# Optimization experiments

Hardware: AMD Instinct MI355X
Metric: run time of the kernel (lower is better)

## Reference

```python
import jax, jax.numpy as jnp
import numpy as np

N = 8192      # total nodes
B = 8         # graphs in batch
L = 1024      # nodes per graph (max_len)
E = 262144    # edges (before self loops)
IN = 64       # in_channels
H = 8         # heads
C = 32        # hidden_channels (per-head out dim)
D = H * C     # 256, d_model
DFF = 2048    # transformer FFN dim (torch default)
NEG = -1e9


def setup_inputs() -> dict:
    key = jax.random.key(0)
    ks = jax.random.split(key, 24)
    def p(i, shape):
        return jax.random.normal(ks[i], shape, jnp.float32) * 0.02
    x = jax.random.normal(ks[0], (N, IN), jnp.float32)
    src = jax.random.randint(ks[1], (E,), 0, N)
    dst = (src // L) * L + jax.random.randint(ks[2], (E,), 0, L)  # keep edges within a graph
    edge_index = jnp.stack([src, dst]).astype(jnp.int32)
    batch = (jnp.arange(N) // L).astype(jnp.int32)
    return dict(
        x=x, edge_index=edge_index, batch=batch,
        gat_W0=p(3, (D, IN)), gat_W12=p(4, (2, D, D)),
        gat_att_src=p(5, (3, H, C)), gat_att_dst=p(6, (3, H, C)), gat_bias=p(7, (3, D)),
        tf_qkv_w=p(8, (2, 3 * D, D)), tf_qkv_b=p(9, (2, 3 * D)),
        tf_out_w=p(10, (2, D, D)), tf_out_b=p(11, (2, D)),
        tf_ln1_w=jnp.ones((2, D)), tf_ln1_b=jnp.zeros((2, D)),
        tf_ln2_w=jnp.ones((2, D)), tf_ln2_b=jnp.zeros((2, D)),
        tf_ff1_w=p(12, (2, DFF, D)), tf_ff1_b=p(13, (2, DFF)),
        tf_ff2_w=p(14, (2, D, DFF)), tf_ff2_b=p(15, (2, D)),
        pred_w=p(16, (3, D)), pred_b=p(17, (3,)),
    )


def _gat(x, src, dst, W, att_s, att_d, bias):
    # PyG GATConv, concat=True, add_self_loops (appended in caller), eval (no dropout)
    h = (x @ W.T).reshape(-1, H, C)                       # [N,H,C]
    a_s = (h * att_s).sum(-1)                             # [N,H]
    a_d = (h * att_d).sum(-1)
    e = jax.nn.leaky_relu(a_s[src] + a_d[dst], 0.2)       # [E+N,H]
    m = jax.ops.segment_max(e, dst, num_segments=N)       # per-dst softmax
    e = jnp.exp(e - m[dst])
    s = jax.ops.segment_sum(e, dst, num_segments=N)
    alpha = e / s[dst]
    out = jax.ops.segment_sum(h[src] * alpha[..., None], dst, num_segments=N)
    return out.reshape(-1, D) + bias


def _ln(x, w, b):
    mu = x.mean(-1, keepdims=True)
    v = ((x - mu) ** 2).mean(-1, keepdims=True)
    return (x - mu) / jnp.sqrt(v + 1e-5) * w + b


def _tf_layer(x, mask, qkv_w, qkv_b, out_w, out_b, ln1w, ln1b, ln2w, ln2b, f1w, f1b, f2w, f2b):
    # torch TransformerEncoderLayer (post-LN, relu), key padding mask, eval mode
    qkv = x @ qkv_w.T + qkv_b                              # [B,L,3D]
    q, k, v = jnp.split(qkv, 3, -1)
    sh = lambda t: t.reshape(B, L, H, D // H)
    q, k, v = sh(q), sh(k), sh(v)
    sc = jnp.einsum('bqhd,bkhd->bhqk', q, k) * (1.0 / float(np.sqrt(D // H)))
    sc = jnp.where(mask[:, None, None, :], NEG, sc)
    a = jax.nn.softmax(sc, -1)
    o = jnp.einsum('bhqk,bkhd->bqhd', a, v).reshape(B, L, D)
    x = _ln(x + o @ out_w.T + out_b, ln1w, ln1b)
    f = jax.nn.relu(x @ f1w.T + f1b) @ f2w.T + f2b
    return _ln(x + f, ln2w, ln2b)


def reference(x, edge_index, batch, gat_W0, gat_W12, gat_att_src, gat_att_dst, gat_bias,
              tf_qkv_w, tf_qkv_b, tf_out_w, tf_out_b, tf_ln1_w, tf_ln1_b, tf_ln2_w, tf_ln2_b,
              tf_ff1_w, tf_ff1_b, tf_ff2_w, tf_ff2_b, pred_w, pred_b):
    loops = jnp.arange(N, dtype=edge_index.dtype)
    src = jnp.concatenate([edge_index[0], loops])
    dst = jnp.concatenate([edge_index[1], loops])
    h = jax.nn.relu(_gat(x, src, dst, gat_W0, gat_att_src[0], gat_att_dst[0], gat_bias[0]))
    for i in range(2):
        h = jax.nn.relu(_gat(h, src, dst, gat_W12[i], gat_att_src[i + 1], gat_att_dst[i + 1], gat_bias[i + 1]))
    # ragged -> padded [B, L, D] (vectorized scatter instead of python loop)
    seq_lens = jax.ops.segment_sum(jnp.ones(N, jnp.int32), batch, num_segments=B)
    starts = jnp.cumsum(seq_lens) - seq_lens
    pos = jnp.arange(N) - starts[batch]
    xp = jnp.zeros((B, L, D), h.dtype).at[batch, pos].set(h)
    mask = jnp.arange(L)[None, :] >= seq_lens[:, None]     # True = padded key
    for i in range(2):
        xp = _tf_layer(xp, mask, tf_qkv_w[i], tf_qkv_b[i], tf_out_w[i], tf_out_b[i],
                       tf_ln1_w[i], tf_ln1_b[i], tf_ln2_w[i], tf_ln2_b[i],
                       tf_ff1_w[i], tf_ff1_b[i], tf_ff2_w[i], tf_ff2_b[i])
    return xp @ pred_w.T + pred_b                          # [B,L,3]
```

## Files before the change

kernel.cpp:

```cpp
#include <hip/hip_runtime.h>
#include <hip/hip_bf16.h>

#define NN 8192
#define EE 262144
#define BB 8
#define LL 1024
#define HH 8
#define DD 256
#define DFFN 2048

typedef short s8v __attribute__((ext_vector_type(8)));
typedef float f32x4 __attribute__((ext_vector_type(4)));
typedef unsigned short ushort;

__device__ inline ushort f2bf(float f) {
    unsigned u = __float_as_uint(f);
    u = (u + 0x7fffu + ((u >> 16) & 1u)) >> 16;
    return (ushort)u;
}
__device__ inline float bf2f(ushort u) {
    return __uint_as_float(((unsigned)u) << 16);
}

__global__ __launch_bounds__(256) void mgemm_ff1_kernel(
    const ushort* __restrict__ A, const ushort* __restrict__ W,
    const float* __restrict__ bias, ushort* __restrict__ Cb,
    int M, int N, int K)
{
    __shared__ ushort As[2][128 * 64];
    __shared__ ushort Bs[2][128 * 64];
    int t = threadIdx.x;
    int l = t & 63;
    int quad = l >> 4, l15 = l & 15;
    int r7 = l15 & 7;
    int w = t >> 6;
    int wm = (w >> 1) * 64, wn = (w & 1) * 64;
    int m0 = blockIdx.x * 128, n0 = blockIdx.y * 128;

    int goffA[4], goffB[4], lo[4];
#pragma unroll
    for (int i = 0; i < 4; ++i) {
        int chunk = i * 256 + t;
        int r = chunk >> 3, p = chunk & 7;
        int qs = (p ^ (r & 7)) * 8;
        goffA[i] = (m0 + r) * K + qs;
        goffB[i] = (n0 + r) * K + qs;
        lo[i] = chunk * 8;
    }

#define STAGE_F(k0, bf)                                                         \
    {                                                                           \
        _Pragma("unroll")                                                       \
        for (int i = 0; i < 4; ++i) {                                           \
            __builtin_amdgcn_global_load_lds(                                   \
                (const __attribute__((address_space(1))) unsigned int*)         \
                    (A + goffA[i] + (k0)),                                      \
                (__attribute__((address_space(3))) unsigned int*)(&As[bf][0] + lo[i]), 16, 0, 0); \
            __builtin_amdgcn_global_load_lds(                                   \
                (const __attribute__((address_space(1))) unsigned int*)         \
                    (W + goffB[i] + (k0)),                                      \
                (__attribute__((address_space(3))) unsigned int*)(&Bs[bf][0] + lo[i]), 16, 0, 0); \
        }                                                                       \
    }

    f32x4 z = {0.f, 0.f, 0.f, 0.f};
    f32x4 acc[4][4];
#pragma unroll
    for (int i = 0; i < 4; ++i)
#pragma unroll
        for (int j = 0; j < 4; ++j) acc[i][j] = z;

    int nt = K >> 6;
    STAGE_F(0, 0);
    for (int ks = 0; ks < nt; ++ks) {
        int cur = ks & 1;
        if (ks + 1 < nt) {
            STAGE_F((ks + 1) << 6, cur ^ 1);
            asm volatile("s_waitcnt vmcnt(8)" ::: "memory");
        } else {
            asm volatile("s_waitcnt vmcnt(0)" ::: "memory");
        }
        __builtin_amdgcn_s_barrier();
        __builtin_amdgcn_sched_barrier(0);
#pragma unroll
        for (int kk = 0; kk < 2; ++kk) {
            int off = ((kk * 4 + quad) ^ r7) * 8;
            s8v af[4], bfv[4];
#pragma unroll
            for (int i = 0; i < 4; ++i) {
                af[i]  = *(const s8v*)(&As[cur][0] + (wm + i * 16 + l15) * 64 + off);
                bfv[i] = *(const s8v*)(&Bs[cur][0] + (wn + i * 16 + l15) * 64 + off);
            }
#pragma unroll
            for (int mi = 0; mi < 4; ++mi)
#pragma unroll
                for (int ni = 0; ni < 4; ++ni)
                    acc[mi][ni] = __builtin_amdgcn_mfma_f32_16x16x32_bf16(
                        af[mi], bfv[ni], acc[mi][ni], 0, 0, 0);
        }
        __builtin_amdgcn_sched_barrier(0);
        __builtin_amdgcn_s_barrier();
    }
#undef STAGE_F

#pragma unroll
    for (int mi = 0; mi < 4; ++mi) {
#pragma unroll
        for (int ni = 0; ni < 4; ++ni) {
            int n = n0 + wn + ni * 16 + l15;
            float bi = bias[n];
#pragma unroll
            for (int r = 0; r < 4; ++r) {
                int m = m0 + wm + mi * 16 + quad * 4 + r;
                float v = fmaxf(acc[mi][ni][r] + bi, 0.f);
                Cb[(size_t)m * N + n] = f2bf(v);
            }
        }
    }
}

template<bool ASD>
__global__ __launch_bounds__(256) void mgemm64_kernel(
    const ushort* __restrict__ A, const ushort* __restrict__ W,
    ushort* __restrict__ Cb,
    const float* __restrict__ atts, const float* __restrict__ attd,
    float* __restrict__ a_s, float* __restrict__ a_d, int M, int N, int K)
{
    __shared__ ushort As[64 * 64];
    __shared__ ushort Bs[64 * 64];
    int t = threadIdx.x;
    int l = t & 63;
    int quad = l >> 4, l15 = l & 15;
    int r7 = l15 & 7;
    int w = t >> 6;
    int wm = (w >> 1) * 32, wn = (w & 1) * 32;
    int m0 = blockIdx.x * 64, n0 = blockIdx.y * 64;

    f32x4 z = {0.f, 0.f, 0.f, 0.f};
    f32x4 acc[2][2];
#pragma unroll
    for (int i = 0; i < 2; ++i)
#pragma unroll
        for (int j = 0; j < 2; ++j) acc[i][j] = z;

    for (int k0 = 0; k0 < K; k0 += 64) {
#pragma unroll
        for (int i = 0; i < 2; ++i) {
            int chunk = i * 256 + t;
            int r = chunk >> 3, p = chunk & 7;
            int qs = (p ^ (r & 7)) * 8;
            __builtin_amdgcn_global_load_lds(
                (const __attribute__((address_space(1))) unsigned int*)
                    (A + (size_t)(m0 + r) * K + k0 + qs),
                (__attribute__((address_space(3))) unsigned int*)(As + chunk * 8), 16, 0, 0);
            __builtin_amdgcn_global_load_lds(
                (const __attribute__((address_space(1))) unsigned int*)
                    (W + (size_t)(n0 + r) * K + k0 + qs),
                (__attribute__((address_space(3))) unsigned int*)(Bs + chunk * 8), 16, 0, 0);
        }
        __syncthreads();
#pragma unroll
        for (int kk = 0; kk < 2; ++kk) {
            s8v af[2], bfv[2];
            int off = ((kk * 4 + quad) ^ r7) * 8;
#pragma unroll
            for (int i = 0; i < 2; ++i) {
                af[i]  = *(const s8v*)(As + (wm + i * 16 + l15) * 64 + off);
                bfv[i] = *(const s8v*)(Bs + (wn + i * 16 + l15) * 64 + off);
            }
#pragma unroll
            for (int mi = 0; mi < 2; ++mi)
#pragma unroll
                for (int ni = 0; ni < 2; ++ni)
                    acc[mi][ni] = __builtin_amdgcn_mfma_f32_16x16x32_bf16(
                        af[mi], bfv[ni], acc[mi][ni], 0, 0, 0);
        }
        __syncthreads();
    }

#pragma unroll
    for (int mi = 0; mi < 2; ++mi) {
#pragma unroll
        for (int ni = 0; ni < 2; ++ni) {
            int n = n0 + wn + ni * 16 + l15;
#pragma unroll
            for (int r = 0; r < 4; ++r) {
                int m = m0 + wm + mi * 16 + quad * 4 + r;
                Cb[(size_t)m * N + n] = f2bf(acc[mi][ni][r]);
            }
        }
    }

    if (ASD) {
        int head = ((n0 + wn) >> 5) & 7;
        float as0 = atts[head * 32 + l15];
        float as1 = atts[head * 32 + 16 + l15];
        float ad0 = attd[head * 32 + l15];
        float ad1 = attd[head * 32 + 16 + l15];
#pragma unroll
        for (int mi = 0; mi < 2; ++mi)
#pragma unroll
            for (int r = 0; r < 4; ++r) {
                float sp = acc[mi][0][r] * as0 + acc[mi][1][r] * as1;
                float dp = acc[mi][0][r] * ad0 + acc[mi][1][r] * ad1;
#pragma unroll
                for (int off = 1; off < 16; off <<= 1) {
                    sp += __shfl_xor(sp, off);
                    dp += __shfl_xor(dp, off);
                }
                if (l15 == 0) {
                    int m = m0 + wm + mi * 16 + quad * 4 + r;
                    a_s[m * 8 + head] = sp;
                    a_d[m * 8 + head] = dp;
                }
            }
    }
}

__global__ __launch_bounds__(256) void gemm0_scatter_kernel(
    const ushort* __restrict__ A, const ushort* __restrict__ W,
    ushort* __restrict__ Cb,
    const float* __restrict__ atts, const float* __restrict__ attd,
    float* __restrict__ a_s, float* __restrict__ a_d,
    const int* __restrict__ ei, int* __restrict__ deg, int* __restrict__ col)
{
    __shared__ ushort As[64 * 64];
    __shared__ ushort Bs[64 * 64];
    int t = threadIdx.x;

    if (blockIdx.x >= 512) {
        int e = (blockIdx.x - 512) * 256 + t;
        if (e < EE + NN) {
            int s, d;
            if (e < EE) { s = ei[e]; d = ei[EE + e]; } else { s = e - EE; d = s; }
            int slot = atomicAdd(&deg[d], 1);
            col[(d << 7) + slot] = s;
        }
        return;
    }

    int l = t & 63;
    int quad = l >> 4, l15 = l & 15;
    int r7 = l15 & 7;
    int w = t >> 6;
    int wm = (w >> 1) * 32, wn = (w & 1) * 32;
    int m0 = (blockIdx.x & 127) * 64, n0 = (blockIdx.x >> 7) * 64;
    const int K = 64;

    f32x4 z = {0.f, 0.f, 0.f, 0.f};
    f32x4 acc[2][2];
#pragma unroll
    for (int i = 0; i < 2; ++i)
#pragma unroll
        for (int j = 0; j < 2; ++j) acc[i][j] = z;

#pragma unroll
    for (int i = 0; i < 2; ++i) {
        int chunk = i * 256 + t;
        int r = chunk >> 3, p = chunk & 7;
        int qs = (p ^ (r & 7)) * 8;
        __builtin_amdgcn_global_load_lds(
            (const __attribute__((address_space(1))) unsigned int*)
                (A + (size_t)(m0 + r) * K + qs),
            (__attribute__((address_space(3))) unsigned int*)(As + chunk * 8), 16, 0, 0);
        __builtin_amdgcn_global_load_lds(
            (const __attribute__((address_space(1))) unsigned int*)
                (W + (size_t)(n0 + r) * K + qs),
            (__attribute__((address_space(3))) unsigned int*)(Bs + chunk * 8), 16, 0, 0);
    }
    __syncthreads();
#pragma unroll
    for (int kk = 0; kk < 2; ++kk) {
        s8v af[2], bfv[2];
        int off = ((kk * 4 + quad) ^ r7) * 8;
#pragma unroll
        for (int i = 0; i < 2; ++i) {
            af[i]  = *(const s8v*)(As + (wm + i * 16 + l15) * 64 + off);
            bfv[i] = *(const s8v*)(Bs + (wn + i * 16 + l15) * 64 + off);
        }
#pragma unroll
        for (int mi = 0; mi < 2; ++mi)
#pragma unroll
            for (int ni = 0; ni < 2; ++ni)
                acc[mi][ni] = __builtin_amdgcn_mfma_f32_16x16x32_bf16(
                    af[mi], bfv[ni], acc[mi][ni], 0, 0, 0);
    }

#pragma unroll
    for (int mi = 0; mi < 2; ++mi) {
#pragma unroll
        for (int ni = 0; ni < 2; ++ni) {
            int n = n0 + wn + ni * 16 + l15;
#pragma unroll
            for (int r = 0; r < 4; ++r) {
                int m = m0 + wm + mi * 16 + quad * 4 + r;
                Cb[(size_t)m * DD + n] = f2bf(acc[mi][ni][r]);
            }
        }
    }

    {
        int head = ((n0 + wn) >> 5) & 7;
        float as0 = atts[head * 32 + l15];
        float as1 = atts[head * 32 + 16 + l15];
        float ad0 = attd[head * 32 + l15];
        float ad1 = attd[head * 32 + 16 + l15];
#pragma unroll
        for (int mi = 0; mi < 2; ++mi)
#pragma unroll
            for (int r = 0; r < 4; ++r) {
                float sp = acc[mi][0][r] * as0 + acc[mi][1][r] * as1;
                float dp = acc[mi][0][r] * ad0 + acc[mi][1][r] * ad1;
#pragma unroll
                for (int off = 1; off < 16; off <<= 1) {
                    sp += __shfl_xor(sp, off);
                    dp += __shfl_xor(dp, off);
                }
                if (l15 == 0) {
                    int m = m0 + wm + mi * 16 + quad * 4 + r;
                    a_s[m * 8 + head] = sp;
                    a_d[m * 8 + head] = dp;
                }
            }
    }
}

template<bool PRED>
__global__ __launch_bounds__(512) void mgemm_ln_kernel(
    const ushort* __restrict__ A, const ushort* __restrict__ W,
    const float* __restrict__ bias, const float* __restrict__ res,
    const float* __restrict__ lnw, const float* __restrict__ lnbb,
    float* __restrict__ Xf, ushort* __restrict__ Xb,
    const float* __restrict__ pw, const float* __restrict__ pb,
    float* __restrict__ pout, int M, int K)
{
    __shared__ ushort As[2][32 * 64];
    __shared__ ushort Bs[2][256 * 64];
    __shared__ float red[2][4][32];
    __shared__ float predred[4][32][3];

    int t = threadIdx.x;
    int l = t & 63;
    int quad = l >> 4, l15 = l & 15;
    int r7 = l15 & 7;
    int w = t >> 6;
    int mh = w >> 2;
    int cw = w & 3;
    int n0w = cw * 64;
    int m0 = blockIdx.x * 32;

    int goffB[4], loB[4];
#pragma unroll
    for (int i = 0; i < 4; ++i) {
        int chunk = i * 512 + t;
        int r = chunk >> 3, p = chunk & 7;
        goffB[i] = r * K + (p ^ (r & 7)) * 8;
        loB[i] = chunk * 8;
    }
    int rA = t >> 3, pA = t & 7;
    int goffA = (m0 + rA) * K + (pA ^ (rA & 7)) * 8;
    int loA = t * 8;

#define STAGE_LN(k0, bf)                                                        \
    {                                                                           \
        _Pragma("unroll")                                                       \
        for (int i = 0; i < 4; ++i)                                             \
            __builtin_amdgcn_global_load_lds(                                   \
                (const __attribute__((address_space(1))) unsigned int*)         \
                    (W + goffB[i] + (k0)),                                      \
                (__attribute__((address_space(3))) unsigned int*)(&Bs[bf][0] + loB[i]), 16, 0, 0); \
        if (t < 256)                                                            \
            __builtin_amdgcn_global_load_lds(                                   \
                (const __attribute__((address_space(1))) unsigned int*)         \
                    (A + goffA + (k0)),                                         \
                (__attribute__((address_space(3))) unsigned int*)(&As[bf][0] + loA), 16, 0, 0); \
    }

    f32x4 z = {0.f, 0.f, 0.f, 0.f};
    f32x4 acc[4];
#pragma unroll
    for (int i = 0; i < 4; ++i) acc[i] = z;

    int nt = K >> 6;
    STAGE_LN(0, 0);
    for (int ks = 0; ks < nt; ++ks) {
        int cur = ks & 1;
        if (ks + 1 < nt) {
            STAGE_LN((ks + 1) << 6, cur ^ 1);
            if (w < 4) { asm volatile("s_waitcnt vmcnt(5)" ::: "memory"); }
            else       { asm volatile("s_waitcnt vmcnt(4)" ::: "memory"); }
        } else {
            asm volatile("s_waitcnt vmcnt(0)" ::: "memory");
        }
        __builtin_amdgcn_s_barrier();
        __builtin_amdgcn_sched_barrier(0);
#pragma unroll
        for (int kk = 0; kk < 2; ++kk) {
            int off = ((kk * 4 + quad) ^ r7) * 8;
            s8v af = *(const s8v*)(&As[cur][0] + (mh * 16 + l15) * 64 + off);
#pragma unroll
            for (int ni = 0; ni < 4; ++ni) {
                s8v bfv = *(const s8v*)(&Bs[cur][0] + (n0w + ni * 16 + l15) * 64 + off);
                acc[ni] = __builtin_amdgcn_mfma_f32_16x16x32_bf16(af, bfv, acc[ni], 0, 0, 0);
            }
        }
        __builtin_amdgcn_sched_barrier(0);
        __builtin_amdgcn_s_barrier();
    }
#undef STAGE_LN

    float v[4][4];
#pragma unroll
    for (int ni = 0; ni < 4; ++ni) {
        int n = n0w + ni * 16 + l15;
        float bi = bias[n];
#pragma unroll
        for (int r = 0; r < 4; ++r) {
            int m = m0 + mh * 16 + quad * 4 + r;
            v[ni][r] = acc[ni][r] + bi + res[(size_t)m * DD + n];
        }
    }
    float s1[4], s2[4];
#pragma unroll
    for (int r = 0; r < 4; ++r) {
        s1[r] = 0.f; s2[r] = 0.f;
#pragma unroll
        for (int ni = 0; ni < 4; ++ni) { s1[r] += v[ni][r]; s2[r] += v[ni][r] * v[ni][r]; }
#pragma unroll
        for (int off = 1; off < 16; off <<= 1) {
            s1[r] += __shfl_xor(s1[r], off);
            s2[r] += __shfl_xor(s2[r], off);
        }
    }
    if (l15 == 0)
#pragma unroll
        for (int r = 0; r < 4; ++r) {
            int row = mh * 16 + quad * 4 + r;
            red[0][cw][row] = s1[r];
            red[1][cw][row] = s2[r];
        }
    __syncthreads();
    float mu[4], rstd[4];
#pragma unroll
    for (int r = 0; r < 4; ++r) {
        int row = mh * 16 + quad * 4 + r;
        float S1 = red[0][0][row] + red[0][1][row] + red[0][2][row] + red[0][3][row];
        float S2 = red[1][0][row] + red[1][1][row] + red[1][2][row] + red[1][3][row];
        mu[r] = S1 * (1.f / 256.f);
        float var = S2 * (1.f / 256.f) - mu[r] * mu[r];
        rstd[r] = rsqrtf(fmaxf(var, 0.f) + 1e-5f);
    }

    float ov[4][4];
#pragma unroll
    for (int ni = 0; ni < 4; ++ni) {
        int n = n0w + ni * 16 + l15;
        float wl = lnw[n], bl = lnbb[n];
#pragma unroll
        for (int r = 0; r < 4; ++r)
            ov[ni][r] = (v[ni][r] - mu[r]) * rstd[r] * wl + bl;
    }

    if (PRED) {
        float ps[3][4] = {};
#pragma unroll
        for (int ni = 0; ni < 4; ++ni) {
            int n = n0w + ni * 16 + l15;
            float w0 = pw[n], w1 = pw[DD + n], w2 = pw[2 * DD + n];
#pragma unroll
            for (int r = 0; r < 4; ++r) {
                ps[0][r] += ov[ni][r] * w0;
                ps[1][r] += ov[ni][r] * w1;
                ps[2][r] += ov[ni][r] * w2;
            }
        }
#pragma unroll
        for (int o3 = 0; o3 < 3; ++o3)
#pragma unroll
            for (int r = 0; r < 4; ++r)
#pragma unroll
                for (int off = 1; off < 16; off <<= 1)
                    ps[o3][r] += __shfl_xor(ps[o3][r], off);
        if (l15 == 0)
#pragma unroll
            for (int o3 = 0; o3 < 3; ++o3)
#pragma unroll
                for (int r = 0; r < 4; ++r)
                    predred[cw][mh * 16 + quad * 4 + r][o3] = ps[o3][r];
        __syncthreads();
        if (t < 96) {
            int row = t / 3, o3 = t % 3;
            float s = predred[0][row][o3] + predred[1][row][o3]
                    + predred[2][row][o3] + predred[3][row][o3] + pb[o3];
            pout[(size_t)(m0 + row) * 3 + o3] = s;
        }
    } else {
#pragma unroll
        for (int ni = 0; ni < 4; ++ni) {
            int n = n0w + ni * 16 + l15;
#pragma unroll
            for (int r = 0; r < 4; ++r) {
                int m = m0 + mh * 16 + quad * 4 + r;
                Xf[(size_t)m * DD + n] = ov[ni][r];
                Xb[(size_t)m * DD + n] = f2bf(ov[ni][r]);
            }
        }
    }
}

__global__ __launch_bounds__(256) void mgemm_qkv_kernel(
    const ushort* __restrict__ A, const ushort* __restrict__ W,
    const float* __restrict__ bias,
    ushort* __restrict__ Qb, ushort* __restrict__ Kb, ushort* __restrict__ Vt,
    int M, int K)
{
    __shared__ ushort As[64 * 64];
    __shared__ ushort Bs[64 * 64];
    __shared__ ushort Vts[64][72];
    int t = threadIdx.x;
    int l = t & 63;
    int quad = l >> 4, l15 = l & 15;
    int r7 = l15 & 7;
    int w = t >> 6;
    int wm = (w >> 1) * 32, wn = (w & 1) * 32;
    int m0 = blockIdx.x * 64, n0 = blockIdx.y * 64;

    f32x4 z = {0.f, 0.f, 0.f, 0.f};
    f32x4 acc[2][2];
#pragma unroll
    for (int i = 0; i < 2; ++i)
#pragma unroll
        for (int j = 0; j < 2; ++j) acc[i][j] = z;

    for (int k0 = 0; k0 < K; k0 += 64) {
#pragma unroll
        for (int i = 0; i < 2; ++i) {
            int chunk = i * 256 + t;
            int r = chunk >> 3, p = chunk & 7;
            int qs = (p ^ (r & 7)) * 8;
            __builtin_amdgcn_global_load_lds(
                (const __attribute__((address_space(1))) unsigned int*)
                    (A + (size_t)(m0 + r) * K + k0 + qs),
                (__attribute__((address_space(3))) unsigned int*)(As + chunk * 8), 16, 0, 0);
            __builtin_amdgcn_global_load_lds(
                (const __attribute__((address_space(1))) unsigned int*)
                    (W + (size_t)(n0 + r) * K + k0 + qs),
                (__attribute__((address_space(3))) unsigned int*)(Bs + chunk * 8), 16, 0, 0);
        }
        __syncthreads();
#pragma unroll
        for (int kk = 0; kk < 2; ++kk) {
            s8v af[2], bfv[2];
            int off = ((kk * 4 + quad) ^ r7) * 8;
#pragma unroll
            for (int i = 0; i < 2; ++i) {
                af[i]  = *(const s8v*)(As + (wm + i * 16 + l15) * 64 + off);
                bfv[i] = *(const s8v*)(Bs + (wn + i * 16 + l15) * 64 + off);
            }
#pragma unroll
            for (int mi = 0; mi < 2; ++mi)
#pragma unroll
                for (int ni = 0; ni < 2; ++ni)
                    acc[mi][ni] = __builtin_amdgcn_mfma_f32_16x16x32_bf16(
                        af[mi], bfv[ni], acc[mi][ni], 0, 0, 0);
        }
        __syncthreads();
    }

    int sec = n0 >> 8;
    if (sec < 2) {
#pragma unroll
        for (int mi = 0; mi < 2; ++mi) {
#pragma unroll
            for (int ni = 0; ni < 2; ++ni) {
                int n = n0 + wn + ni * 16 + l15;
                int hc = n & 255;
                int hh = hc >> 5, c = hc & 31;
                float bv = bias[n];
#pragma unroll
                for (int r = 0; r < 4; ++r) {
                    int m = m0 + wm + mi * 16 + quad * 4 + r;
                    float v = acc[mi][ni][r] + bv;
                    int b = m >> 10, ll2 = m & 1023;
                    int bh = b * 8 + hh;
                    if (sec == 0)
                        Qb[(size_t)bh * 32768 + ll2 * 32 + c] = f2bf(v * 0.17677669529663687f);
                    else
                        Kb[(size_t)bh * 32768 + ll2 * 32 + c] = f2bf(v);
                }
            }
        }
    } else {
#pragma unroll
        for (int mi = 0; mi < 2; ++mi) {
#pragma unroll
            for (int ni = 0; ni < 2; ++ni) {
                int nl = wn + ni * 16 + l15;
                float bv = bias[n0 + nl];
#pragma unroll
                for (int r = 0; r < 4; ++r) {
                    int ml = wm + mi * 16 + quad * 4 + r;
                    Vts[nl][ml] = f2bf(acc[mi][ni][r] + bv);
                }
            }
        }
        __syncthreads();
        int b = m0 >> 10;
        int ll2base = m0 & 1023;
#pragma unroll
        for (int it = 0; it < 2; ++it) {
            int chunk = it * 256 + t;
            int nl = chunk >> 3;
            int me = (chunk & 7) * 8;
            int n = n0 + nl;
            int hh = (n & 255) >> 5, c = n & 31;
            ushort* dst = Vt + (size_t)(b * 8 + hh) * 32768 + (size_t)c * 1024 + ll2base + me;
            *(s8v*)dst = *(const s8v*)&Vts[nl][me];
        }
    }
}

__global__ __launch_bounds__(256) void castall_kernel(
    const float* __restrict__ W0, const float* __restrict__ W12,
    const float* __restrict__ qkvw, const float* __restrict__ outw,
    const float* __restrict__ f1w, const float* __restrict__ f2w,
    const float* __restrict__ x,
    ushort* __restrict__ W0b, ushort* __restrict__ W12b,
    ushort* __restrict__ qkvb, ushort* __restrict__ outb,
    ushort* __restrict__ f1b, ushort* __restrict__ f2b,
    ushort* __restrict__ xb, int* __restrict__ deg)
{
    int tid = blockIdx.x * 256 + threadIdx.x;
    if (tid < 2048) *(int4*)(deg + tid * 4) = make_int4(0, 0, 0, 0);
    int e = tid * 4;
    if (e >= 3293184) return;
    const float* s; ushort* d; int off;
    if (e < 16384)        { s = W0;   d = W0b;  off = e; }
    else if (e < 147456)  { s = W12;  d = W12b; off = e - 16384; }
    else if (e < 540672)  { s = qkvw; d = qkvb; off = e - 147456; }
    else if (e < 671744)  { s = outw; d = outb; off = e - 540672; }
    else if (e < 1720320) { s = f1w;  d = f1b;  off = e - 671744; }
    else if (e < 2768896) { s = f2w;  d = f2b;  off = e - 1720320; }
    else                  { s = x;    d = xb;   off = e - 2768896; }
    float4 v = *(const float4*)(s + off);
    d[off + 0] = f2bf(v.x); d[off + 1] = f2bf(v.y);
    d[off + 2] = f2bf(v.z); d[off + 3] = f2bf(v.w);
}

template<bool WF>
__global__ __launch_bounds__(256) void gat_agg_kernel(
    const ushort* __restrict__ hlinb, const float* __restrict__ a_s,
    const float* __restrict__ a_d, const int* __restrict__ deg,
    const int* __restrict__ col, const float* __restrict__ bias,
    float* __restrict__ out, ushort* __restrict__ outb)
{
    int wid = threadIdx.x >> 6, lane = threadIdx.x & 63;
    int dst = blockIdx.x * 4 + wid;
    int start = dst << 7;
    int end = start + deg[dst];
    int myh = lane >> 3;
    float adh = a_d[(size_t)dst * HH + myh];

    float a0 = 0.f, a1 = 0.f, a2 = 0.f, a3 = 0.f, den = 0.f;
    int e = start;
    for (; e + 4 <= end; e += 4) {
        int s0 = col[e], s1 = col[e + 1], s2 = col[e + 2], s3 = col[e + 3];
        float v0 = a_s[(size_t)s0 * HH + myh] + adh;
        float v1 = a_s[(size_t)s1 * HH + myh] + adh;
        float v2 = a_s[(size_t)s2 * HH + myh] + adh;
        float v3 = a_s[(size_t)s3 * HH + myh] + adh;
        v0 = v0 > 0.f ? v0 : 0.2f * v0;
        v1 = v1 > 0.f ? v1 : 0.2f * v1;
        v2 = v2 > 0.f ? v2 : 0.2f * v2;
        v3 = v3 > 0.f ? v3 : 0.2f * v3;
        float p0 = __expf(v0), p1 = __expf(v1), p2 = __expf(v2), p3 = __expf(v3);
        den += p0 + p1 + p2 + p3;
        uint2 h0 = *(const uint2*)(hlinb + (size_t)s0 * DD + lane * 4);
        uint2 h1 = *(const uint2*)(hlinb + (size_t)s1 * DD + lane * 4);
        uint2 h2 = *(const uint2*)(hlinb + (size_t)s2 * DD + lane * 4);
        uint2 h3 = *(const uint2*)(hlinb + (size_t)s3 * DD + lane * 4);
        a0 += p0 * bf2f((ushort)(h0.x & 0xffff)) + p1 * bf2f((ushort)(h1.x & 0xffff))
            + p2 * bf2f((ushort)(h2.x & 0xffff)) + p3 * bf2f((ushort)(h3.x & 0xffff));
        a1 += p0 * bf2f((ushort)(h0.x >> 16)) + p1 * bf2f((ushort)(h1.x >> 16))
            + p2 * bf2f((ushort)(h2.x >> 16)) + p3 * bf2f((ushort)(h3.x >> 16));
        a2 += p0 * bf2f((ushort)(h0.y & 0xffff)) + p1 * bf2f((ushort)(h1.y & 0xffff))
            + p2 * bf2f((ushort)(h2.y & 0xffff)) + p3 * bf2f((ushort)(h3.y & 0xffff));
        a3 += p0 * bf2f((ushort)(h0.y >> 16)) + p1 * bf2f((ushort)(h1.y >> 16))
            + p2 * bf2f((ushort)(h2.y >> 16)) + p3 * bf2f((ushort)(h3.y >> 16));
    }
    for (; e < end; ++e) {
        int s = col[e];
        float v = a_s[(size_t)s * HH + myh] + adh;
        v = v > 0.f ? v : 0.2f * v;
        float p = __expf(v);
        den += p;
        uint2 hv = *(const uint2*)(hlinb + (size_t)s * DD + lane * 4);
        a0 += p * bf2f((ushort)(hv.x & 0xffff));
        a1 += p * bf2f((ushort)(hv.x >> 16));
        a2 += p * bf2f((ushort)(hv.y & 0xffff));
        a3 += p * bf2f((ushort)(hv.y >> 16));
    }
    float inv = 1.f / den;
    float4 bv = *(const float4*)(bias + lane * 4);
    float r0 = fmaxf(a0 * inv + bv.x, 0.f);
    float r1 = fmaxf(a1 * inv + bv.y, 0.f);
    float r2 = fmaxf(a2 * inv + bv.z, 0.f);
    float r3 = fmaxf(a3 * inv + bv.w, 0.f);
    if (WF) {
        float* op = out + (size_t)dst * DD + lane * 4;
        op[0] = r0; op[1] = r1; op[2] = r2; op[3] = r3;
    }
    ushort* ob = outb + (size_t)dst * DD + lane * 4;
    ob[0] = f2bf(r0); ob[1] = f2bf(r1); ob[2] = f2bf(r2); ob[3] = f2bf(r3);
}

__global__ __launch_bounds__(256, 2) void attn_flash_kernel(
    const ushort* __restrict__ Qb, const ushort* __restrict__ Kb,
    const ushort* __restrict__ Vt, ushort* __restrict__ outb)
{
    __shared__ ushort Ks[2][128 * 32];
    __shared__ ushort Vs[2][32 * 128];
    __shared__ ushort pw[4][32][132];

    int t = threadIdx.x;
    int w = t >> 6, lane = t & 63;
    int quad = lane >> 4, l15 = lane & 15;
    int kq = (quad ^ ((l15 >> 1) & 3)) * 8;
    int bh = blockIdx.y;
    int q0 = blockIdx.x * 128 + w * 32;
    int b = bh >> 3, h = bh & 7;

    const ushort* qbase = Qb + (size_t)bh * 32768;
    const ushort* kbase = Kb + (size_t)bh * 32768;
    const ushort* vbase = Vt + (size_t)bh * 32768;

    s8v aq0 = *(const s8v*)(qbase + (q0 + l15) * 32 + quad * 8);
    s8v aq1 = *(const s8v*)(qbase + (q0 + 16 + l15) * 32 + quad * 8);

    s8v vone;
#pragma unroll
    for (int i = 0; i < 8; ++i) vone[i] = (short)0x3F80;

    int i0 = t, i1 = 256 + t;
    int kr0 = i0 >> 2, kcs0 = (((i0 & 3)) ^ ((kr0 >> 1) & 3)) * 8;
    int kr1 = i1 >> 2, kcs1 = (((i1 & 3)) ^ ((kr1 >> 1) & 3)) * 8;
    int vr0 = i0 >> 4, vcs0 = ((i0 & 15) ^ (vr0 & 15)) * 8;
    int vr1 = i1 >> 4, vcs1 = ((i1 & 15) ^ (vr1 & 15)) * 8;

#define STAGE(ch, bf)                                                          \
    {                                                                          \
        int j0 = (ch) * 128;                                                   \
        __builtin_amdgcn_global_load_lds(                                      \
            (const __attribute__((address_space(1))) unsigned int*)            \
                (kbase + (size_t)(j0 + kr0) * 32 + kcs0),                      \
            (__attribute__((address_space(3))) unsigned int*)(Ks[bf] + i0 * 8), 16, 0, 0); \
        __builtin_amdgcn_global_load_lds(                                      \
            (const __attribute__((address_space(1))) unsigned int*)            \
                (kbase + (size_t)(j0 + kr1) * 32 + kcs1),                      \
            (__attribute__((address_space(3))) unsigned int*)(Ks[bf] + i1 * 8), 16, 0, 0); \
        __builtin_amdgcn_global_load_lds(                                      \
            (const __attribute__((address_space(1))) unsigned int*)            \
                (vbase + (size_t)vr0 * 1024 + j0 + vcs0),                      \
            (__attribute__((address_space(3))) unsigned int*)(Vs[bf] + i0 * 8), 16, 0, 0); \
        __builtin_amdgcn_global_load_lds(                                      \
            (const __attribute__((address_space(1))) unsigned int*)            \
                (vbase + (size_t)vr1 * 1024 + j0 + vcs1),                      \
            (__attribute__((address_space(3))) unsigned int*)(Vs[bf] + i1 * 8), 16, 0, 0); \
    }

    f32x4 z = {0.f, 0.f, 0.f, 0.f};
    f32x4 o00 = z, o01 = z, o10 = z, o11 = z;
    f32x4 od0 = z, od1 = z;

    STAGE(0, 0);
    for (int ch = 0; ch < 8; ++ch) {
        int bf = ch & 1;
        __syncthreads();
        if (ch < 7) STAGE(ch + 1, bf ^ 1);

        f32x4 s0[8], s1[8];
#pragma unroll
        for (int kk = 0; kk < 8; ++kk) {
            s8v bk = *(const s8v*)(Ks[bf] + (kk * 16 + l15) * 32 + kq);
            s0[kk] = __builtin_amdgcn_mfma_f32_16x16x32_bf16(aq0, bk, z, 0, 0, 0);
            s1[kk] = __builtin_amdgcn_mfma_f32_16x16x32_bf16(aq1, bk, z, 0, 0, 0);
        }

#pragma unroll
        for (int kk = 0; kk < 8; ++kk) {
#pragma unroll
            for (int r = 0; r < 4; ++r) {
                float p0 = __expf(s0[kk][r]);
                float p1 = __expf(s1[kk][r]);
                pw[w][quad * 4 + r][kk * 16 + l15]      = f2bf(p0);
                pw[w][16 + quad * 4 + r][kk * 16 + l15] = f2bf(p1);
            }
        }

#pragma unroll
        for (int kk = 0; kk < 4; ++kk) {
            s8v ap0 = *(const s8v*)(&pw[w][l15][kk * 32 + quad * 8]);
            s8v ap1 = *(const s8v*)(&pw[w][16 + l15][kk * 32 + quad * 8]);
            int c0 = ((kk * 4 + quad) ^ l15) * 8;
            s8v b0 = *(const s8v*)(Vs[bf] + (size_t)l15 * 128 + c0);
            s8v b1 = *(const s8v*)(Vs[bf] + (size_t)(16 + l15) * 128 + c0);
            o00 = __builtin_amdgcn_mfma_f32_16x16x32_bf16(ap0, b0, o00, 0, 0, 0);
            o01 = __builtin_amdgcn_mfma_f32_16x16x32_bf16(ap0, b1, o01, 0, 0, 0);
            o10 = __builtin_amdgcn_mfma_f32_16x16x32_bf16(ap1, b0, o10, 0, 0, 0);
            o11 = __builtin_amdgcn_mfma_f32_16x16x32_bf16(ap1, b1, o11, 0, 0, 0);
            od0 = __builtin_amdgcn_mfma_f32_16x16x32_bf16(ap0, vone, od0, 0, 0, 0);
            od1 = __builtin_amdgcn_mfma_f32_16x16x32_bf16(ap1, vone, od1, 0, 0, 0);
        }
    }
#undef STAGE

#pragma unroll
    for (int r = 0; r < 4; ++r) {
        int row0 = q0 + quad * 4 + r;
        int row1 = row0 + 16;
        float i0v = 1.f / od0[r];
        float i1v = 1.f / od1[r];
        outb[(size_t)(b * 1024 + row0) * 256 + h * 32 + l15]      = f2bf(o00[r] * i0v);
        outb[(size_t)(b * 1024 + row0) * 256 + h * 32 + 16 + l15] = f2bf(o01[r] * i0v);
        outb[(size_t)(b * 1024 + row1) * 256 + h * 32 + l15]      = f2bf(o10[r] * i1v);
        outb[(size_t)(b * 1024 + row1) * 256 + h * 32 + 16 + l15] = f2bf(o11[r] * i1v);
    }
}

extern "C" void kernel_launch(void* const* d_in, const int* in_sizes, int n_in,
                              void* d_out, int out_size, void* d_ws, size_t ws_size,
                              hipStream_t stream)
{
    const float* x        = (const float*)d_in[0];
    const int*   ei       = (const int*)d_in[1];
    const float* gat_W0   = (const float*)d_in[3];
    const float* gat_W12  = (const float*)d_in[4];
    const float* att_src  = (const float*)d_in[5];
    const float* att_dst  = (const float*)d_in[6];
    const float* gat_bias = (const float*)d_in[7];
    const float* qkv_w    = (const float*)d_in[8];
    const float* qkv_b    = (const float*)d_in[9];
    const float* out_w    = (const float*)d_in[10];
    const float* out_b    = (const float*)d_in[11];
    const float* ln1_w    = (const float*)d_in[12];
    const float* ln1_b    = (const float*)d_in[13];
    const float* ln2_w    = (const float*)d_in[14];
    const float* ln2_b    = (const float*)d_in[15];
    const float* ff1_w    = (const float*)d_in[16];
    const float* ff1_b    = (const float*)d_in[17];
    const float* ff2_w    = (const float*)d_in[18];
    const float* ff2_b    = (const float*)d_in[19];
    const float* pred_w   = (const float*)d_in[20];
    const float* pred_b   = (const float*)d_in[21];
    float* outp = (float*)d_out;

    float* ws   = (float*)d_ws;
    float* hA   = ws;
    float* hB   = ws + 2097152;
    ushort* ffb  = (ushort*)(ws + 4194304);
    ushort* Qb   = (ushort*)(ws + 12582912);
    ushort* Kb   = (ushort*)(ws + 13631488);
    ushort* Vt   = (ushort*)(ws + 14680064);
    ushort* attnb= (ushort*)(ws + 15728640);
    ushort* lnb  = (ushort*)(ws + 16777216);
    ushort* hBb  = (ushort*)(ws + 17825792);
    ushort* xb   = (ushort*)(ws + 18874368);
    ushort* wbase= (ushort*)(ws + 19136512);
    ushort* W0b    = wbase;
    ushort* W12b   = wbase + 16384;
    ushort* qkv_wb = wbase + 147456;
    ushort* out_wb = wbase + 540672;
    ushort* ff1_wb = wbase + 671744;
    ushort* ff2_wb = wbase + 1720320;
    float* a_s  = ws + 20520960;
    float* a_d  = ws + 20586496;
    int*   deg  = (int*)(ws + 20652032);
    ushort* hAb    = (ushort*)(ws + 21000192);
    int*   col  = (int*)(ws + 30437376);

    castall_kernel<<<3216, 256, 0, stream>>>(
        gat_W0, gat_W12, qkv_w, out_w, ff1_w, ff2_w, x,
        W0b, W12b, qkv_wb, out_wb, ff1_wb, ff2_wb, xb, deg);

    gemm0_scatter_kernel<<<1568, 256, 0, stream>>>(
        xb, W0b, hAb, att_src, att_dst, a_s, a_d, ei, deg, col);
    gat_agg_kernel<false><<<2048, 256, 0, stream>>>(
        hAb, a_s, a_d, deg, col, gat_bias, nullptr, hBb);

    for (int l = 0; l < 2; ++l) {
        mgemm64_kernel<true><<<dim3(128, 4), 256, 0, stream>>>(
            hBb, W12b + (size_t)l * DD * DD, hAb,
            att_src + (l + 1) * 256, att_dst + (l + 1) * 256, a_s, a_d, NN, DD, DD);
        if (l == 0)
            gat_agg_kernel<false><<<2048, 256, 0, stream>>>(
                hAb, a_s, a_d, deg, col, gat_bias + 256, nullptr, hBb);
        else
            gat_agg_kernel<true><<<2048, 256, 0, stream>>>(
                hAb, a_s, a_d, deg, col, gat_bias + 512, hB, hBb);
    }

    for (int l = 0; l < 2; ++l) {
        mgemm_qkv_kernel<<<dim3(128, 12), 256, 0, stream>>>(
            hBb, qkv_wb + (size_t)l * 768 * DD, qkv_b + l * 768, Qb, Kb, Vt, NN, DD);
        attn_flash_kernel<<<dim3(8, 64), 256, 0, stream>>>(Qb, Kb, Vt, attnb);
        mgemm_ln_kernel<false><<<256, 512, 0, stream>>>(
            attnb, out_wb + (size_t)l * DD * DD, out_b + l * DD, hB,
            ln1_w + l * DD, ln1_b + l * DD, hA, lnb,
            nullptr, nullptr, nullptr, NN, DD);
        mgemm_ff1_kernel<<<dim3(64, 16), 256, 0, stream>>>(
            lnb, ff1_wb + (size_t)l * DFFN * DD, ff1_b + l * DFFN, ffb, NN, DFFN, DD);
        if (l == 0) {
            mgemm_ln_kernel<false><<<256, 512, 0, stream>>>(
                ffb, ff2_wb, ff2_b, hA,
                ln2_w, ln2_b, hB, hBb,
                nullptr, nullptr, nullptr, NN, DFFN);
        } else {
            mgemm_ln_kernel<true><<<256, 512, 0, stream>>>(
                ffb, ff2_wb + (size_t)DD * DFFN, ff2_b + DD, hA,
                ln2_w + DD, ln2_b + DD, nullptr, nullptr,
                pred_w, pred_b, outp, NN, DFFN);
        }
    }
}
```

Measured before the change: 378.8 us.

## Fuse transformer FFN up-projection, ReLU, down-projection and LayerNorm into one kernel

Replaces the separate FF1 GEMM (writing an 8192x2048 bf16 intermediate) and the FF2+LayerNorm GEMM with a single kernel. Each block owns 32 rows and streams 64-column chunks of W1 and W2 through double-buffered LDS. It computes the ReLU activations into LDS and accumulates the down-projection in registers, so the large intermediate never goes to global memory. The cost is that each 32-row block re-reads the full W1/W2 weights. Only 256 blocks run, each with small MFMA tiles and two barriers per chunk, which may lower MFMA utilisation compared with the 128x128 tiled GEMMs.

Measured after the change: 386.0 us. About the same (+1.9%).

```diff
diff --git a/kernel.cpp b/kernel.cpp
--- a/kernel.cpp
+++ b/kernel.cpp
@@ -22,98 +22,222 @@
     return __uint_as_float(((unsigned)u) << 16);
 }
 
-__global__ __launch_bounds__(256) void mgemm_ff1_kernel(
-    const ushort* __restrict__ A, const ushort* __restrict__ W,
-    const float* __restrict__ bias, ushort* __restrict__ Cb,
-    int M, int N, int K)
+template<bool PRED>
+__global__ __launch_bounds__(512) void ffn_fused_kernel(
+    const ushort* __restrict__ A, const ushort* __restrict__ W1,
+    const float* __restrict__ b1, const ushort* __restrict__ W2,
+    const float* __restrict__ b2, const float* __restrict__ res,
+    const float* __restrict__ lnw, const float* __restrict__ lnbb,
+    float* __restrict__ Xf, ushort* __restrict__ Xb,
+    const float* __restrict__ pw, const float* __restrict__ pb,
+    float* __restrict__ pout)
 {
-    __shared__ ushort As[2][128 * 64];
-    __shared__ ushort Bs[2][128 * 64];
+    __shared__ ushort xs[32 * 256];
+    __shared__ ushort w1s[2][64 * 256];
+    __shared__ ushort w2s[2][256 * 64];
+    __shared__ float  b1s[2][64];
+    __shared__ ushort acts[32 * 64];
+    __shared__ float red[2][4][32];
+    __shared__ float predred[4][32][3];
+
     int t = threadIdx.x;
     int l = t & 63;
     int quad = l >> 4, l15 = l & 15;
     int r7 = l15 & 7;
     int w = t >> 6;
-    int wm = (w >> 1) * 64, wn = (w & 1) * 64;
-    int m0 = blockIdx.x * 128, n0 = blockIdx.y * 128;
-
-    int goffA[4], goffB[4], lo[4];
+    int rt = w >> 2;
+    int ct = w & 3;
+    int m0 = blockIdx.x * 32;
+
+#pragma unroll
+    for (int it = 0; it < 2; ++it) {
+        int ck = it * 512 + t;
+        int r = ck >> 5, g = ck & 31;
+        __builtin_amdgcn_global_load_lds(
+            (const __attribute__((address_space(1))) unsigned int*)
+                (A + (size_t)(m0 + r) * 256 + (g >> 3) * 64 + ((g & 7) ^ (r & 7)) * 8),
+            (__attribute__((address_space(3))) unsigned int*)(xs + ck * 8), 16, 0, 0);
+    }
+
+    int o1[4], o2[4], lo[4];
 #pragma unroll
     for (int i = 0; i < 4; ++i) {
-        int chunk = i * 256 + t;
-        int r = chunk >> 3, p = chunk & 7;
-        int qs = (p ^ (r & 7)) * 8;
-        goffA[i] = (m0 + r) * K + qs;
-        goffB[i] = (n0 + r) * K + qs;
-        lo[i] = chunk * 8;
-    }
-
-#define STAGE_F(k0, bf)                                                         \
-    {                                                                           \
-        _Pragma("unroll")                                                       \
-        for (int i = 0; i < 4; ++i) {                                           \
-            __builtin_amdgcn_global_load_lds(                                   \
-                (const __attribute__((address_space(1))) unsigned int*)         \
-                    (A + goffA[i] + (k0)),                                      \
-                (__attribute__((address_space(3))) unsigned int*)(&As[bf][0] + lo[i]), 16, 0, 0); \
-            __builtin_amdgcn_global_load_lds(                                   \
-                (const __attribute__((address_space(1))) unsigned int*)         \
-                    (W + goffB[i] + (k0)),                                      \
-                (__attribute__((address_space(3))) unsigned int*)(&Bs[bf][0] + lo[i]), 16, 0, 0); \
-        }                                                                       \
+        int ck = i * 512 + t;
+        int r1 = ck >> 5, g1 = ck & 31;
+        o1[i] = r1 * 256 + (g1 >> 3) * 64 + ((g1 & 7) ^ (r1 & 7)) * 8;
+        int r2 = ck >> 3, p2 = ck & 7;
+        o2[i] = r2 * 2048 + ((p2 ^ (r2 & 7)) * 8);
+        lo[i] = ck * 8;
+    }
+
+#define STAGE_W(nb, bf)                                                        \
+    {                                                                          \
+        _Pragma("unroll")                                                      \
+        for (int i = 0; i < 4; ++i) {                                          \
+            __builtin_amdgcn_global_load_lds(                                  \
+                (const __attribute__((address_space(1))) unsigned int*)        \
+                    (W1 + (size_t)(nb) * 16384 + o1[i]),                       \
+                (__attribute__((address_space(3))) unsigned int*)(&w1s[bf][0] + lo[i]), 16, 0, 0); \
+            __builtin_amdgcn_global_load_lds(                                  \
+                (const __attribute__((address_space(1))) unsigned int*)        \
+                    (W2 + (size_t)(nb) * 64 + o2[i]),                          \
+                (__attribute__((address_space(3))) unsigned int*)(&w2s[bf][0] + lo[i]), 16, 0, 0); \
+        }                                                                      \
+        if (t < 16)                                                            \
+            __builtin_amdgcn_global_load_lds(                                  \
+                (const __attribute__((address_space(1))) unsigned int*)        \
+                    (b1 + (nb) * 64 + t * 4),                                  \
+                (__attribute__((address_space(3))) unsigned int*)(&b1s[bf][0] + t * 4), 16, 0, 0); \
     }
 
     f32x4 z = {0.f, 0.f, 0.f, 0.f};
-    f32x4 acc[4][4];
-#pragma unroll
-    for (int i = 0; i < 4; ++i)
-#pragma unroll
-        for (int j = 0; j < 4; ++j) acc[i][j] = z;
-
-    int nt = K >> 6;
-    STAGE_F(0, 0);
-    for (int ks = 0; ks < nt; ++ks) {
-        int cur = ks & 1;
-        if (ks + 1 < nt) {
-            STAGE_F((ks + 1) << 6, cur ^ 1);
-            asm volatile("s_waitcnt vmcnt(8)" ::: "memory");
+    f32x4 acc2[4];
+#pragma unroll
+    for (int i = 0; i < 4; ++i) acc2[i] = z;
+
+    STAGE_W(0, 0);
+    for (int nb = 0; nb < 32; ++nb) {
+        int cur = nb & 1;
+        if (nb + 1 < 32) {
+            STAGE_W(nb + 1, cur ^ 1);
+            if (w == 0) { asm volatile("s_waitcnt vmcnt(9)" ::: "memory"); }
+            else        { asm volatile("s_waitcnt vmcnt(8)" ::: "memory"); }
         } else {
             asm volatile("s_waitcnt vmcnt(0)" ::: "memory");
         }
         __builtin_amdgcn_s_barrier();
         __builtin_amdgcn_sched_barrier(0);
-#pragma unroll
-        for (int kk = 0; kk < 2; ++kk) {
-            int off = ((kk * 4 + quad) ^ r7) * 8;
-            s8v af[4], bfv[4];
-#pragma unroll
-            for (int i = 0; i < 4; ++i) {
-                af[i]  = *(const s8v*)(&As[cur][0] + (wm + i * 16 + l15) * 64 + off);
-                bfv[i] = *(const s8v*)(&Bs[cur][0] + (wn + i * 16 + l15) * 64 + off);
-            }
-#pragma unroll
-            for (int mi = 0; mi < 4; ++mi)
-#pragma unroll
-                for (int ni = 0; ni < 4; ++ni)
-                    acc[mi][ni] = __builtin_amdgcn_mfma_f32_16x16x32_bf16(
-                        af[mi], bfv[ni], acc[mi][ni], 0, 0, 0);
-        }
+
+        f32x4 aa = z;
+#pragma unroll
+        for (int kk = 0; kk < 8; ++kk) {
+            int off = (kk >> 1) * 64 + (((kk & 1) * 4 + quad) ^ r7) * 8;
+            s8v af  = *(const s8v*)(xs + (rt * 16 + l15) * 256 + off);
+            s8v bfv = *(const s8v*)(&w1s[cur][0] + (ct * 16 + l15) * 256 + off);
+            aa = __builtin_amdgcn_mfma_f32_16x16x32_bf16(af, bfv, aa, 0, 0, 0);
+        }
+        float bia = b1s[cur][ct * 16 + l15];
+        int cc = ct * 16 + l15;
+        int qc = cc >> 3, ec = cc & 7;
+#pragma unroll
+        for (int r = 0; r < 4; ++r) {
+            int m = rt * 16 + quad * 4 + r;
+            float v = fmaxf(aa[r] + bia, 0.f);
+            acts[m * 64 + ((qc ^ (m & 7)) * 8) + ec] = f2bf(v);
+        }
+        asm volatile("s_waitcnt lgkmcnt(0)" ::: "memory");
         __builtin_amdgcn_sched_barrier(0);
         __builtin_amdgcn_s_barrier();
-    }
-#undef STAGE_F
-
-#pragma unroll
-    for (int mi = 0; mi < 4; ++mi) {
-#pragma unroll
-        for (int ni = 0; ni < 4; ++ni) {
-            int n = n0 + wn + ni * 16 + l15;
-            float bi = bias[n];
+        __builtin_amdgcn_sched_barrier(0);
+
+#pragma unroll
+        for (int kk2 = 0; kk2 < 2; ++kk2) {
+            int off = ((kk2 * 4 + quad) ^ r7) * 8;
+            s8v af2 = *(const s8v*)(acts + (rt * 16 + l15) * 64 + off);
+#pragma unroll
+            for (int ot = 0; ot < 4; ++ot) {
+                s8v bf2 = *(const s8v*)(&w2s[cur][0] + (ct * 64 + ot * 16 + l15) * 64 + off);
+                acc2[ot] = __builtin_amdgcn_mfma_f32_16x16x32_bf16(af2, bf2, acc2[ot], 0, 0, 0);
+            }
+        }
+        __builtin_amdgcn_sched_barrier(0);
+        __builtin_amdgcn_s_barrier();
+    }
+#undef STAGE_W
+
+    float vv[4][4];
+#pragma unroll
+    for (int ot = 0; ot < 4; ++ot) {
+        int o = ct * 64 + ot * 16 + l15;
+        float bo = b2[o];
+#pragma unroll
+        for (int r = 0; r < 4; ++r) {
+            int m = m0 + rt * 16 + quad * 4 + r;
+            vv[ot][r] = acc2[ot][r] + bo + res[(size_t)m * DD + o];
+        }
+    }
+    float s1[4], s2[4];
+#pragma unroll
+    for (int r = 0; r < 4; ++r) {
+        s1[r] = 0.f; s2[r] = 0.f;
+#pragma unroll
+        for (int ot = 0; ot < 4; ++ot) { s1[r] += vv[ot][r]; s2[r] += vv[ot][r] * vv[ot][r]; }
+#pragma unroll
+        for (int off = 1; off < 16; off <<= 1) {
+            s1[r] += __shfl_xor(s1[r], off);
+            s2[r] += __shfl_xor(s2[r], off);
+        }
+    }
+    if (l15 == 0)
+#pragma unroll
+        for (int r = 0; r < 4; ++r) {
+            int row = rt * 16 + quad * 4 + r;
+            red[0][ct][row] = s1[r];
+            red[1][ct][row] = s2[r];
+        }
+    __syncthreads();
+    float mu[4], rstd[4];
+#pragma unroll
+    for (int r = 0; r < 4; ++r) {
+        int row = rt * 16 + quad * 4 + r;
+        float S1 = red[0][0][row] + red[0][1][row] + red[0][2][row] + red[0][3][row];
+        float S2 = red[1][0][row] + red[1][1][row] + red[1][2][row] + red[1][3][row];
+        mu[r] = S1 * (1.f / 256.f);
+        float var = S2 * (1.f / 256.f) - mu[r] * mu[r];
+        rstd[r] = rsqrtf(fmaxf(var, 0.f) + 1e-5f);
+    }
+    float ov[4][4];
+#pragma unroll
+    for (int ot = 0; ot < 4; ++ot) {
+        int o = ct * 64 + ot * 16 + l15;
+        float wl = lnw[o], bl = lnbb[o];
+#pragma unroll
+        for (int r = 0; r < 4; ++r)
+            ov[ot][r] = (vv[ot][r] - mu[r]) * rstd[r] * wl + bl;
+    }
+
+    if (PRED) {
+        float ps[3][4] = {};
+#pragma unroll
+        for (int ot = 0; ot < 4; ++ot) {
+            int o = ct * 64 + ot * 16 + l15;
+            float w0 = pw[o], w1v = pw[DD + o], w2v = pw[2 * DD + o];
 #pragma unroll
             for (int r = 0; r < 4; ++r) {
-                int m = m0 + wm + mi * 16 + quad * 4 + r;
-                float v = fmaxf(acc[mi][ni][r] + bi, 0.f);
-                Cb[(size_t)m * N + n] = f2bf(v);
+                ps[0][r] += ov[ot][r] * w0;
+                ps[1][r] += ov[ot][r] * w1v;
+                ps[2][r] += ov[ot][r] * w2v;
+            }
+        }
+#pragma unroll
+        for (int o3 = 0; o3 < 3; ++o3)
+#pragma unroll
+            for (int r = 0; r < 4; ++r)
+#pragma unroll
+                for (int off = 1; off < 16; off <<= 1)
+                    ps[o3][r] += __shfl_xor(ps[o3][r], off);
+        if (l15 == 0)
+#pragma unroll
+            for (int o3 = 0; o3 < 3; ++o3)
+#pragma unroll
+                for (int r = 0; r < 4; ++r)
+                    predred[ct][rt * 16 + quad * 4 + r][o3] = ps[o3][r];
+        __syncthreads();
+        if (t < 96) {
+            int row = t / 3, o3 = t % 3;
+            float s = predred[0][row][o3] + predred[1][row][o3]
+                    + predred[2][row][o3] + predred[3][row][o3] + pb[o3];
+            pout[(size_t)(m0 + row) * 3 + o3] = s;
+        }
+    } else {
+#pragma unroll
+        for (int ot = 0; ot < 4; ++ot) {
+            int o = ct * 64 + ot * 16 + l15;
+#pragma unroll
+            for (int r = 0; r < 4; ++r) {
+                int m = m0 + rt * 16 + quad * 4 + r;
+                Xf[(size_t)m * DD + o] = ov[ot][r];
+                Xb[(size_t)m * DD + o] = f2bf(ov[ot][r]);
             }
         }
     }
@@ -857,7 +981,6 @@
     float* ws   = (float*)d_ws;
     float* hA   = ws;
     float* hB   = ws + 2097152;
-    ushort* ffb  = (ushort*)(ws + 4194304);
     ushort* Qb   = (ushort*)(ws + 12582912);
     ushort* Kb   = (ushort*)(ws + 13631488);
     ushort* Vt   = (ushort*)(ws + 14680064);
@@ -907,18 +1030,16 @@
             attnb, out_wb + (size_t)l * DD * DD, out_b + l * DD, hB,
             ln1_w + l * DD, ln1_b + l * DD, hA, lnb,
             nullptr, nullptr, nullptr, NN, DD);
-        mgemm_ff1_kernel<<<dim3(64, 16), 256, 0, stream>>>(
-            lnb, ff1_wb + (size_t)l * DFFN * DD, ff1_b + l * DFFN, ffb, NN, DFFN, DD);
         if (l == 0) {
-            mgemm_ln_kernel<false><<<256, 512, 0, stream>>>(
-                ffb, ff2_wb, ff2_b, hA,
-                ln2_w, ln2_b, hB, hBb,
-                nullptr, nullptr, nullptr, NN, DFFN);
+            ffn_fused_kernel<false><<<256, 512, 0, stream>>>(
+                lnb, ff1_wb, ff1_b, ff2_wb, ff2_b, hA,
+                ln2_w, ln2_b, hB, hBb, nullptr, nullptr, nullptr);
         } else {
-            mgemm_ln_kernel<true><<<256, 512, 0, stream>>>(
-                ffb, ff2_wb + (size_t)DD * DFFN, ff2_b + DD, hA,
+            ffn_fused_kernel<true><<<256, 512, 0, stream>>>(
+                lnb, ff1_wb + (size_t)DFFN * DD, ff1_b + DFFN,
+                ff2_wb + (size_t)DD * DFFN, ff2_b + DD, hA,
                 ln2_w + DD, ln2_b + DD, nullptr, nullptr,
-                pred_w, pred_b, outp, NN, DFFN);
+                pred_w, pred_b, outp);
         }
     }
 }
```
